# Performance work log

Hardware: AMD Instinct MI355X
Metric: run time of the kernel (lower is better)

## Reference

```python
import jax, jax.numpy as jnp
import numpy as np

EPS = 1e-6
R_ROTS = 3
MAX_DEG = 4.0
MD = 1  # max_disp_z = max_disp_y = max_disp_x = 1
E = (2 * MD + 1) ** 3  # 27


def eul2rotm_y(ry):
    # rotation about the y axis (rx = rz = 0 in the original eul2rotm call)
    c, s = jnp.cos(ry), jnp.sin(ry)
    z, o = jnp.zeros_like(ry), jnp.ones_like(ry)
    return jnp.stack([jnp.stack([c, z, s], -1),
                      jnp.stack([z, o, z], -1),
                      jnp.stack([-s, z, c], -1)], -2)  # [N,3,3]


def merge_rt(r, t):
    N = r.shape[0]
    top = jnp.concatenate([r, t[:, :, None]], axis=2)
    bot = jnp.broadcast_to(jnp.array([[[0.0, 0.0, 0.0, 1.0]]], dtype=r.dtype), (N, 1, 4))
    return jnp.concatenate([top, bot], axis=1)  # [N,4,4]


def invert_rt(rt):
    r = rt[:, :3, :3]
    t = rt[:, :3, 3]
    rinv = jnp.swapaxes(r, 1, 2)
    tinv = -jnp.einsum('nij,nj->ni', rinv, t)
    return merge_rt(rinv, tinv)


def trilinear_sample(vox, xyz):
    # vox [N,C,Z,Y,X]; xyz [N,Z,Y,X,3] voxel-space (x,y,z) coords; zero outside
    N, C, Z, Y, X = vox.shape
    x, y, z = xyz[..., 0], xyz[..., 1], xyz[..., 2]
    x0, y0, z0 = jnp.floor(x), jnp.floor(y), jnp.floor(z)
    fx, fy, fz = x - x0, y - y0, z - z0
    voxf = vox.reshape(N, C, Z * Y * X)
    gather = jax.vmap(lambda v, i: v[:, i])  # per-batch gather over flat spatial
    out = jnp.zeros((N, C, Z, Y, X), vox.dtype)
    for dz in (0, 1):
        wz = fz if dz else (1.0 - fz)
        zc = z0 + dz
        for dy in (0, 1):
            wy = fy if dy else (1.0 - fy)
            yc = y0 + dy
            for dx in (0, 1):
                wx = fx if dx else (1.0 - fx)
                xc = x0 + dx
                valid = ((xc >= 0) & (xc <= X - 1) & (yc >= 0) & (yc <= Y - 1)
                         & (zc >= 0) & (zc <= Z - 1))
                xi = jnp.clip(xc, 0, X - 1).astype(jnp.int32)
                yi = jnp.clip(yc, 0, Y - 1).astype(jnp.int32)
                zi = jnp.clip(zc, 0, Z - 1).astype(jnp.int32)
                idx = (zi * Y + yi) * X + xi  # [N,Z,Y,X]
                vals = gather(voxf, idx.reshape(N, -1)).reshape(N, C, Z, Y, X)
                w = (wx * wy * wz * valid.astype(vox.dtype))[:, None]
                out = out + w * vals
    return out


def apply_4x4_to_vox(T, vox):
    # warp vox by rigid transform T (unit voxel size, grid-centered Mem2Ref)
    N, C, Z, Y, X = vox.shape
    Tinv = invert_rt(T)
    zz, yy, xx = jnp.meshgrid(jnp.arange(Z), jnp.arange(Y), jnp.arange(X), indexing='ij')
    grid = jnp.stack([xx, yy, zz], -1).astype(vox.dtype)  # [Z,Y,X,3] in (x,y,z)
    center = (jnp.array([X, Y, Z], vox.dtype) - 1.0) / 2.0
    ref = grid - center
    src = jnp.einsum('nij,zyxj->nzyxi', Tinv[:, :3, :3], ref) + Tinv[:, None, None, None, :3, 3]
    return trilinear_sample(vox, src + center)


def cost_volume_3d(v0, v1):
    # masked-mean correlation over C for every shift in a 3x3x3 neighborhood
    N, C, D, H, W = v0.shape
    v1p = jnp.pad(v1, ((0, 0), (0, 0), (MD, MD), (MD, MD), (MD, MD)))
    mask = jnp.pad(jnp.ones((N, 1, D, H, W), v0.dtype),
                   ((0, 0), (0, 0), (MD, MD), (MD, MD), (MD, MD)))
    costs = []
    for dz in range(2 * MD + 1):
        for dy in range(2 * MD + 1):
            for dx in range(2 * MD + 1):
                sl = v1p[:, :, dz:dz + D, dy:dy + H, dx:dx + W]
                m = mask[:, :, dz:dz + D, dy:dy + H, dx:dx + W]
                num = jnp.sum(v0 * sl, axis=1, keepdims=True)
                den = m * C  # sum of mask broadcast over C channels
                costs.append(num / (den + EPS))
    return jnp.concatenate(costs, axis=1)  # [N,27,D,H,W]


def setup_inputs() -> dict:
    key = jax.random.key(0)
    ks = jax.random.split(key, 8)
    B, C, Z, Y, X = 4, 32, 64, 32, 64
    feat0 = jax.random.normal(ks[0], (B, C, Z, Y, X), jnp.float32)
    feat1 = jax.random.normal(ks[1], (B, C, Z, Y, X), jnp.float32)
    ry_g = jax.random.uniform(ks[2], (B,), jnp.float32, -0.05, 0.05)
    t_g = 0.5 * jax.random.normal(ks[3], (B, 3), jnp.float32)
    cam0_T_cam1_g = merge_rt(eul2rotm_y(ry_g), t_g)
    fan = R_ROTS * E  # 81
    W1 = jax.random.normal(ks[4], (128, fan), jnp.float32) / np.sqrt(fan)
    b1 = jnp.zeros((128,), jnp.float32)
    W2 = jax.random.normal(ks[5], (128, 128), jnp.float32) / np.sqrt(128.0)
    b2 = jnp.zeros((128,), jnp.float32)
    W3 = jax.random.normal(ks[6], (4, 128), jnp.float32) / np.sqrt(128.0)
    b3 = jnp.zeros((4,), jnp.float32)
    return dict(feat0=feat0, feat1=feat1, cam0_T_cam1_g=cam0_T_cam1_g,
                W1=W1, b1=b1, W2=W2, b2=b2, W3=W3, b3=b3)


def reference(feat0, feat1, cam0_T_cam1_g, W1, b1, W2, b2, W3, b3):
    B, C, Z, Y, X = feat0.shape
    # candidate y-rotations, replicated per batch element
    rots = jnp.linspace(-MAX_DEG, MAX_DEG, R_ROTS)
    ry = jnp.tile(rots[None, :], (B, 1)).reshape(B * R_ROTS)
    camN_T_cam1 = merge_rt(eul2rotm_y(jnp.deg2rad(ry)), jnp.zeros((B * R_ROTS, 3), feat0.dtype))
    feat0r = jnp.repeat(feat0[:, None], R_ROTS, axis=1).reshape(B * R_ROTS, C, Z, Y, X)
    feat1r = jnp.repeat(feat1[:, None], R_ROTS, axis=1).reshape(B * R_ROTS, C, Z, Y, X)
    featN = apply_4x4_to_vox(camN_T_cam1, feat1r)
    cc = cost_volume_3d(feat0r, featN)                # [B*R,27,Z,Y,X]
    heat = jnp.sum(cc, axis=(2, 3, 4))                 # [B*R,27]
    f = heat.reshape(B, R_ROTS * E)
    f = jax.nn.leaky_relu(f, 0.1)
    f = f / (EPS + jnp.sqrt(jnp.sum(f * f, axis=1, keepdims=True)))
    f = jax.nn.leaky_relu(f @ W1.T + b1, 0.1)
    f = jax.nn.leaky_relu(f @ W2.T + b2, 0.1)
    f = f @ W3.T + b3                                  # [B,4]
    r_out, yv, xv, zv = f[:, 0], f[:, 1], f[:, 2], f[:, 3]
    # Mem2Ref is affine with unit voxel size -> delta == (x,y,z) directly
    delta = jnp.stack([xv, yv, zv], axis=1)
    cam0_T_cam1_e = merge_rt(eul2rotm_y(jnp.deg2rad(r_out)), -delta)
    feat1_warped = apply_4x4_to_vox(cam0_T_cam1_e, feat1)
    # eval_against_gt (coeffs folded to 1.0, sc=1.0)
    ry_of = lambda rt: jnp.arctan2(rt[:, 0, 2], rt[:, 2, 2])
    deg_e = jnp.rad2deg(ry_of(cam0_T_cam1_e))
    deg_g = jnp.rad2deg(ry_of(cam0_T_cam1_g))
    t_e = cam0_T_cam1_e[:, :3, 3]
    t_g = cam0_T_cam1_g[:, :3, 3]
    t_l2 = jnp.mean(jnp.sum((t_e - t_g) ** 2, axis=1))
    deg_l2 = jnp.mean((deg_e - deg_g) ** 2)
    total_loss = t_l2 + deg_l2
    return total_loss, cam0_T_cam1_e, feat1_warped
```

## Files before the change

### kernel.cpp

```cpp
#include <hip/hip_runtime.h>
#include <math.h>

#define NCH 32
#define CHV (64*32*64)
#define NB 4
#define NT2 512
#define INVC (1.0f/(32.0f+1e-6f))
#define D2R 0.017453292519943295f
#define R2D 57.29577951308232f

#define P1A 73
#define P1B 72
#define F0B (32*P1A)
#define UNITSZ (32*P1A + 24*P1B)

__global__ __launch_bounds__(256) void k_heat(const float* __restrict__ feat0,
                                              const float* __restrict__ feat1,
                                              float* __restrict__ partial)
{
    __shared__ float L[2][UNITSZ];

    const int lid = (int)blockIdx.x;
    const int nid = (lid & 7) * 256 + (lid >> 3);
    const int yt  = nid & 7;
    const int zt  = (nid >> 3) & 31;
    const int chh = (nid >> 8) & 1;
    const int b   = nid >> 9;

    const int tid = (int)threadIdx.x;
    const int wv = tid >> 6;
    const int lane = tid & 63;
    const int tx = lane & 15, ty = lane >> 4;
    const int x0 = 4 * tx;
    const int z0 = 2 * zt;
    const bool ident = (wv == 1);

    const float* f0base = feat0 + ((size_t)b * NCH + chh * 16) * CHV;
    const float* f1base = feat1 + ((size_t)b * NCH + chh * 16) * CHV;

    int aB[2][4];
    float wAx[2][4], wBx[2][4], wZl[2][4];
    if (wv == 0 || wv == 2) {
        const float th = 4.0f * (float)(wv - 1) * D2R;
        const float cs = cosf(th), sn = sinf(th);
        #pragma unroll
        for (int k = 0; k < 2; ++k) {
            #pragma unroll
            for (int i = 0; i < 4; ++i) {
                const float rx = (float)(x0 + i) - 31.5f;
                const float rz = (float)(z0 + k) - 31.5f;
                const float sx = cs * rx - sn * rz + 31.5f;
                const float sz = sn * rx + cs * rz + 31.5f;
                const float xf = floorf(sx), zf = floorf(sz);
                const float fx = sx - xf, fz = sz - zf;
                const int ix = (int)xf, iz = (int)zf;
                int bx; float A_, B_;
                if (ix == -1)      { bx = 0;  A_ = fx;        B_ = 0.0f; }
                else if (ix == 63) { bx = 62; A_ = 0.0f;      B_ = 1.0f - fx; }
                else if ((unsigned)ix <= 62u) { bx = ix; A_ = 1.0f - fx; B_ = fx; }
                else               { bx = 0;  A_ = 0.0f;      B_ = 0.0f; }
                wAx[k][i] = A_; wBx[k][i] = B_;
                wZl[k][i] = 1.0f - fz;
                const int zl = min(max(iz - (2 * zt - 3), 0), 6);
                aB[k][i] = (zl * 4 + ty) * P1A + bx;
            }
        }
    }
    const int iA0 = (12 + ty) * P1A + x0;
    const int iA1 = iA0 + 4 * P1A;
    const int fb0 = F0B + ty * P1B + x0;

    float acc[27];
    #pragma unroll
    for (int o = 0; o < 27; ++o) acc[o] = 0.0f;

#define STAGE_CH(CHN)                                                           \
    {                                                                           \
        const int u_ = (CHN) & 1;                                               \
        const float* f1c_ = f1base + (size_t)(CHN) * CHV;                       \
        const float* f0c_ = f0base + (size_t)(CHN) * CHV;                       \
        float* Ln_ = &L[u_][0];                                                 \
        const int tq_ = lane >> 4, c4_ = (lane & 15) << 2;                      \
        float4 v1_[8], v0_[6];                                                  \
        _Pragma("unroll")                                                       \
        for (int k_ = 0; k_ < 8; ++k_) {                                        \
            const int zs_ = 2 * zt - 3 + k_;                                    \
            v1_[k_] = (float4){0.0f, 0.0f, 0.0f, 0.0f};                         \
            if (zs_ >= 0 && zs_ < 64)                                           \
                v1_[k_] = *(const float4*)(f1c_ + zs_ * 2048                    \
                            + (4 * yt + tq_) * 64 + c4_);                       \
        }                                                                       \
        _Pragma("unroll")                                                       \
        for (int k_ = 0; k_ < 6; ++k_) {                                        \
            const int r_ = 4 * k_ + tq_;                                        \
            const int i_ = (r_ * 43) >> 8;                                      \
            const int j_ = r_ - 6 * i_;                                         \
            const int zf_ = 2 * zt - 1 + i_;                                    \
            const int yf_ = 4 * yt - 1 + j_;                                    \
            v0_[k_] = (float4){0.0f, 0.0f, 0.0f, 0.0f};                         \
            if (zf_ >= 0 && zf_ < 64 && yf_ >= 0 && yf_ < 32)                   \
                v0_[k_] = *(const float4*)(f0c_ + zf_ * 2048 + yf_ * 64 + c4_); \
        }                                                                       \
        _Pragma("unroll")                                                       \
        for (int k_ = 0; k_ < 8; ++k_) {                                        \
            const int w_ = (4 * k_ + tq_) * P1A + c4_;                          \
            Ln_[w_ + 0] = v1_[k_].x; Ln_[w_ + 1] = v1_[k_].y;                   \
            Ln_[w_ + 2] = v1_[k_].z; Ln_[w_ + 3] = v1_[k_].w;                   \
        }                                                                       \
        _Pragma("unroll")                                                       \
        for (int k_ = 0; k_ < 6; ++k_)                                          \
            *(float4*)&Ln_[F0B + (4 * k_ + tq_) * P1B + c4_] = v0_[k_];         \
    }

#define ROWFMA(KK, OZP1, YRI, R)                                                \
    { const int base_ = (OZP1) * 9 + (2 - (YRI)) * 3;                           \
      acc[base_ + 0] += g0[KK]*R.x + fr[KK][0]*R.y + fr[KK][1]*R.z + fr[KK][2]*R.w; \
      acc[base_ + 1] += fr[KK][0]*R.x + fr[KK][1]*R.y + fr[KK][2]*R.z + fr[KK][3]*R.w; \
      acc[base_ + 2] += fr[KK][1]*R.x + fr[KK][2]*R.y + fr[KK][3]*R.z + g5[KK]*R.w; }

    if (wv == 3) STAGE_CH(0)
    __syncthreads();

    #pragma unroll 1
    for (int ch = 0; ch < 16; ++ch) {
        if (wv == 3) {
            if (ch + 1 < 16) STAGE_CH(ch + 1)
        } else {
            const float* Lb = &L[ch & 1][0];

            float fr[2][4];
            if (ident) {
                #pragma unroll
                for (int i = 0; i < 4; ++i) {
                    fr[0][i] = Lb[iA0 + i];
                    fr[1][i] = Lb[iA1 + i];
                }
            } else {
                #pragma unroll
                for (int k = 0; k < 2; ++k) {
                    #pragma unroll
                    for (int i = 0; i < 4; ++i) {
                        const int a = aB[k][i];
                        const float p00 = Lb[a], p01 = Lb[a + 1];
                        const float p10 = Lb[a + 4 * P1A], p11 = Lb[a + 4 * P1A + 1];
                        const float sLo = wAx[k][i] * p00 + wBx[k][i] * p01;
                        const float sHi = wAx[k][i] * p10 + wBx[k][i] * p11;
                        fr[k][i] = sHi + wZl[k][i] * (sLo - sHi);
                    }
                }
            }

            float g0[2], g5[2];
            #pragma unroll
            for (int k = 0; k < 2; ++k) {
                const float a_ = __shfl_up(fr[k][3], 1, 64);
                const float c_ = __shfl_down(fr[k][0], 1, 64);
                g0[k] = (tx == 0) ? 0.0f : a_;
                g5[k] = (tx == 15) ? 0.0f : c_;
            }

            __builtin_amdgcn_s_setprio(1);
            #pragma unroll
            for (int zri = 0; zri < 4; ++zri) {
                const float4 R0 = *(const float4*)&Lb[fb0 + (zri * 6 + 0) * P1B];
                const float4 R1 = *(const float4*)&Lb[fb0 + (zri * 6 + 1) * P1B];
                const float4 R2 = *(const float4*)&Lb[fb0 + (zri * 6 + 2) * P1B];
                if (zri == 0) { ROWFMA(0, 2, 0, R0) ROWFMA(0, 2, 1, R1) ROWFMA(0, 2, 2, R2) }
                if (zri == 1) { ROWFMA(0, 1, 0, R0) ROWFMA(0, 1, 1, R1) ROWFMA(0, 1, 2, R2)
                                ROWFMA(1, 2, 0, R0) ROWFMA(1, 2, 1, R1) ROWFMA(1, 2, 2, R2) }
                if (zri == 2) { ROWFMA(0, 0, 0, R0) ROWFMA(0, 0, 1, R1) ROWFMA(0, 0, 2, R2)
                                ROWFMA(1, 1, 0, R0) ROWFMA(1, 1, 1, R1) ROWFMA(1, 1, 2, R2) }
                if (zri == 3) { ROWFMA(1, 0, 0, R0) ROWFMA(1, 0, 1, R1) ROWFMA(1, 0, 2, R2) }
            }
            __builtin_amdgcn_s_setprio(0);
        }
        __syncthreads();
    }
#undef ROWFMA
#undef STAGE_CH

    if (wv < 3) {
        const int slot = (zt * 8 + yt) * 2 + chh;
        #pragma unroll 1
        for (int o = 0; o < 27; ++o) {
            float v = acc[o];
            #pragma unroll
            for (int d = 32; d >= 1; d >>= 1) v += __shfl_down(v, d, 64);
            if (lane == 0)
                partial[((size_t)((b * 3 + wv) * 27) + o) * NT2 + slot] = v;
        }
    }
}

__global__ __launch_bounds__(128) void k_hsum(const float* __restrict__ partial,
                                              float* __restrict__ heatw)
{
    __shared__ float red[2];
    const int r = (int)blockIdx.x;
    const int tid = (int)threadIdx.x;
    const int lane = tid & 63, wid = tid >> 6;

    const float4 v = ((const float4*)(partial + (size_t)r * NT2))[tid];
    float s = (v.x + v.y) + (v.z + v.w);
    #pragma unroll
    for (int d = 32; d >= 1; d >>= 1) s += __shfl_down(s, d, 64);
    if (lane == 0) red[wid] = s;
    __syncthreads();
    if (tid == 0) heatw[r] = (red[0] + red[1]) * INVC;
}

__global__ __launch_bounds__(128) void k_mlp(const float* __restrict__ heatw,
                                             const float* __restrict__ camg,
                                             const float* __restrict__ W1,
                                             const float* __restrict__ b1,
                                             const float* __restrict__ W2,
                                             const float* __restrict__ b2,
                                             const float* __restrict__ W3,
                                             const float* __restrict__ b3,
                                             float* __restrict__ out,
                                             float* __restrict__ params)
{
    __shared__ float heat[324];
    __shared__ float f[81];
    __shared__ float h1[128];
    __shared__ float h2[128];
    __shared__ float denom_s;
    __shared__ float res[NB][8];
    const int tid = (int)threadIdx.x;

    for (int p = tid; p < 324; p += 128) heat[p] = heatw[p];
    __syncthreads();

    for (int b = 0; b < NB; ++b) {
        if (tid < 81) {
            float v = heat[b * 81 + tid];
            f[tid] = (v >= 0.0f) ? v : 0.1f * v;
        }
        __syncthreads();
        if (tid == 0) {
            float ss = 0.0f;
            for (int k = 0; k < 81; ++k) ss += f[k] * f[k];
            denom_s = 1e-6f + sqrtf(ss);
        }
        __syncthreads();
        if (tid < 81) f[tid] = f[tid] / denom_s;
        __syncthreads();
        {
            float a = b1[tid];
            const float* wr = W1 + tid * 81;
            for (int k = 0; k < 81; ++k) a += wr[k] * f[k];
            h1[tid] = (a >= 0.0f) ? a : 0.1f * a;
        }
        __syncthreads();
        {
            float a = b2[tid];
            const float* wr = W2 + tid * 128;
            for (int k = 0; k < 128; ++k) a += wr[k] * h1[k];
            h2[tid] = (a >= 0.0f) ? a : 0.1f * a;
        }
        __syncthreads();
        if (tid < 4) {
            float a = b3[tid];
            const float* wr = W3 + tid * 128;
            for (int k = 0; k < 128; ++k) a += wr[k] * h2[k];
            res[b][4 + tid] = a;
        }
        __syncthreads();
        if (tid == 0) {
            const float r_out = res[b][4], yv = res[b][5], xv = res[b][6], zv = res[b][7];
            const float t2 = r_out * D2R;
            const float c2 = cosf(t2), s2 = sinf(t2);
            float* m = out + 1 + b * 16;
            m[0] = c2;  m[1] = 0.0f; m[2] = s2;  m[3] = -xv;
            m[4] = 0.0f; m[5] = 1.0f; m[6] = 0.0f; m[7] = -yv;
            m[8] = -s2; m[9] = 0.0f; m[10] = c2; m[11] = -zv;
            m[12] = 0.0f; m[13] = 0.0f; m[14] = 0.0f; m[15] = 1.0f;
            params[b * 8 + 0] = c2;
            params[b * 8 + 1] = s2;
            params[b * 8 + 2] = c2 * xv - s2 * zv;
            params[b * 8 + 3] = yv;
            params[b * 8 + 4] = s2 * xv + c2 * zv;
            res[b][0] = -xv; res[b][1] = -yv; res[b][2] = -zv;
            res[b][3] = atan2f(s2, c2) * R2D;
        }
        __syncthreads();
    }

    if (tid == 0) {
        float tl2 = 0.0f, dl2 = 0.0f;
        for (int b = 0; b < NB; ++b) {
            const float* g = camg + b * 16;
            const float dx = res[b][0] - g[3];
            const float dy = res[b][1] - g[7];
            const float dz = res[b][2] - g[11];
            tl2 += dx * dx + dy * dy + dz * dz;
            const float dg = atan2f(g[2], g[10]) * R2D;
            const float dd = res[b][3] - dg;
            dl2 += dd * dd;
        }
        out[0] = tl2 * 0.25f + dl2 * 0.25f;
    }
}

__global__ __launch_bounds__(256) void k_warp(const float* __restrict__ feat1,
                                              const float* __restrict__ params,
                                              float* __restrict__ outw)
{
    const int b = blockIdx.y;
    const int p = (int)blockIdx.x * 256 + (int)threadIdx.x;
    const int z = p >> 11;
    const int y = (p >> 6) & 31;
    const int x = p & 63;

    const float cs = params[b * 8 + 0], sn = params[b * 8 + 1];
    const float tpx = params[b * 8 + 2], tpy = params[b * 8 + 3], tpz = params[b * 8 + 4];

    const float rx = (float)x - 31.5f;
    const float ry = (float)y - 15.5f;
    const float rz = (float)z - 31.5f;
    const float sx = cs * rx - sn * rz + tpx + 31.5f;
    const float sy = ry + tpy + 15.5f;
    const float sz = sn * rx + cs * rz + tpz + 31.5f;

    const float xf = floorf(sx), yf = floorf(sy), zf = floorf(sz);
    const float fx = sx - xf, fy = sy - yf, fz = sz - zf;
    const int ix = (int)xf, iy = (int)yf, iz = (int)zf;

    const float wx[2] = {1.0f - fx, fx};
    const float wy[2] = {1.0f - fy, fy};
    const float wz[2] = {1.0f - fz, fz};
    const int xs[2] = {min(max(ix, 0), 63), min(max(ix + 1, 0), 63)};
    const int ys[2] = {min(max(iy, 0), 31), min(max(iy + 1, 0), 31)};
    const int zs[2] = {min(max(iz, 0), 63), min(max(iz + 1, 0), 63)};
    const bool vx[2] = {(unsigned)ix < 64u, (unsigned)(ix + 1) < 64u};
    const bool vy[2] = {(unsigned)iy < 32u, (unsigned)(iy + 1) < 32u};
    const bool vz[2] = {(unsigned)iz < 64u, (unsigned)(iz + 1) < 64u};

    int idx[8]; float w[8];
    int q = 0;
    #pragma unroll
    for (int dz = 0; dz < 2; ++dz)
        #pragma unroll
        for (int dy = 0; dy < 2; ++dy)
            #pragma unroll
            for (int dx = 0; dx < 2; ++dx) {
                idx[q] = zs[dz] * 2048 + ys[dy] * 64 + xs[dx];
                w[q] = (vx[dx] && vy[dy] && vz[dz]) ? wx[dx] * wy[dy] * wz[dz] : 0.0f;
                ++q;
            }

    const float* f1b = feat1 + (size_t)b * NCH * CHV;
    float* ob = outw + (size_t)b * NCH * CHV;
    #pragma unroll 2
    for (int c = 0; c < NCH; ++c) {
        const float* f1c = f1b + (size_t)c * CHV;
        float a = 0.0f;
        #pragma unroll
        for (int k = 0; k < 8; ++k) a += w[k] * f1c[idx[k]];
        ob[(size_t)c * CHV + p] = a;
    }
}

extern "C" void kernel_launch(void* const* d_in, const int* in_sizes, int n_in,
                              void* d_out, int out_size, void* d_ws, size_t ws_size,
                              hipStream_t stream)
{
    (void)in_sizes; (void)n_in; (void)out_size; (void)ws_size;
    const float* feat0 = (const float*)d_in[0];
    const float* feat1 = (const float*)d_in[1];
    const float* camg  = (const float*)d_in[2];
    const float* W1 = (const float*)d_in[3];
    const float* b1 = (const float*)d_in[4];
    const float* W2 = (const float*)d_in[5];
    const float* b2 = (const float*)d_in[6];
    const float* W3 = (const float*)d_in[7];
    const float* b3 = (const float*)d_in[8];
    float* out = (float*)d_out;

    float* partial = (float*)d_ws;
    float* params  = partial + 324 * NT2;
    float* heatw   = params + 32;

    hipLaunchKernelGGL(k_heat, dim3(2048), dim3(256), 0, stream,
                       feat0, feat1, partial);
    hipLaunchKernelGGL(k_hsum, dim3(324), dim3(128), 0, stream, partial, heatw);
    hipLaunchKernelGGL(k_mlp, dim3(1), dim3(128), 0, stream,
                       heatw, camg, W1, b1, W2, b2, W3, b3, out, params);
    dim3 g3((64*32*64) / 256, NB);
    hipLaunchKernelGGL(k_warp, g3, dim3(256), 0, stream, feat1, params, out + 65);
}
```

Measured before the change: 192.6 us.

## Fuse heat reduction into per-batch MLP, split loss, vectorize warp

Removes the separate partial-sum reduction kernel and folds it into the MLP kernel, which now runs one block per batch, so the four batches no longer run serially in a single block. The final loss moves into a tiny separate kernel. The warp kernel now handles four consecutive x voxels per thread, writes them with a float4 store, and remaps blocks to spread batches across XCDs. The priority hints around the FMA section of k_heat are also dropped. The per-thread loop over 128 float4 in the MLP block is a serial read that could lengthen that stage.

Result: slower. 274.8 us (+42.7%).

```diff
diff --git a/kernel.cpp b/kernel.cpp
--- a/kernel.cpp
+++ b/kernel.cpp
@@ -159,7 +159,6 @@
                 g5[k] = (tx == 15) ? 0.0f : c_;
             }
 
-            __builtin_amdgcn_s_setprio(1);
             #pragma unroll
             for (int zri = 0; zri < 4; ++zri) {
                 const float4 R0 = *(const float4*)&Lb[fb0 + (zri * 6 + 0) * P1B];
@@ -172,7 +171,6 @@
                                 ROWFMA(1, 1, 0, R0) ROWFMA(1, 1, 1, R1) ROWFMA(1, 1, 2, R2) }
                 if (zri == 3) { ROWFMA(1, 0, 0, R0) ROWFMA(1, 0, 1, R1) ROWFMA(1, 0, 2, R2) }
             }
-            __builtin_amdgcn_s_setprio(0);
         }
         __syncthreads();
     }
@@ -192,25 +190,7 @@
     }
 }
 
-__global__ __launch_bounds__(128) void k_hsum(const float* __restrict__ partial,
-                                              float* __restrict__ heatw)
-{
-    __shared__ float red[2];
-    const int r = (int)blockIdx.x;
-    const int tid = (int)threadIdx.x;
-    const int lane = tid & 63, wid = tid >> 6;
-
-    const float4 v = ((const float4*)(partial + (size_t)r * NT2))[tid];
-    float s = (v.x + v.y) + (v.z + v.w);
-    #pragma unroll
-    for (int d = 32; d >= 1; d >>= 1) s += __shfl_down(s, d, 64);
-    if (lane == 0) red[wid] = s;
-    __syncthreads();
-    if (tid == 0) heatw[r] = (red[0] + red[1]) * INVC;
-}
-
-__global__ __launch_bounds__(128) void k_mlp(const float* __restrict__ heatw,
-                                             const float* __restrict__ camg,
+__global__ __launch_bounds__(128) void k_mlp(const float* __restrict__ partial,
                                              const float* __restrict__ W1,
                                              const float* __restrict__ b1,
                                              const float* __restrict__ W2,
@@ -218,84 +198,93 @@
                                              const float* __restrict__ W3,
                                              const float* __restrict__ b3,
                                              float* __restrict__ out,
-                                             float* __restrict__ params)
-{
-    __shared__ float heat[324];
+                                             float* __restrict__ params,
+                                             float* __restrict__ resv)
+{
     __shared__ float f[81];
     __shared__ float h1[128];
     __shared__ float h2[128];
     __shared__ float denom_s;
-    __shared__ float res[NB][8];
+    __shared__ float r4[4];
+    const int b = (int)blockIdx.x;
     const int tid = (int)threadIdx.x;
 
-    for (int p = tid; p < 324; p += 128) heat[p] = heatw[p];
-    __syncthreads();
-
-    for (int b = 0; b < NB; ++b) {
-        if (tid < 81) {
-            float v = heat[b * 81 + tid];
-            f[tid] = (v >= 0.0f) ? v : 0.1f * v;
-        }
-        __syncthreads();
-        if (tid == 0) {
-            float ss = 0.0f;
-            for (int k = 0; k < 81; ++k) ss += f[k] * f[k];
-            denom_s = 1e-6f + sqrtf(ss);
-        }
-        __syncthreads();
-        if (tid < 81) f[tid] = f[tid] / denom_s;
-        __syncthreads();
-        {
-            float a = b1[tid];
-            const float* wr = W1 + tid * 81;
-            for (int k = 0; k < 81; ++k) a += wr[k] * f[k];
-            h1[tid] = (a >= 0.0f) ? a : 0.1f * a;
-        }
-        __syncthreads();
-        {
-            float a = b2[tid];
-            const float* wr = W2 + tid * 128;
-            for (int k = 0; k < 128; ++k) a += wr[k] * h1[k];
-            h2[tid] = (a >= 0.0f) ? a : 0.1f * a;
-        }
-        __syncthreads();
-        if (tid < 4) {
-            float a = b3[tid];
-            const float* wr = W3 + tid * 128;
-            for (int k = 0; k < 128; ++k) a += wr[k] * h2[k];
-            res[b][4 + tid] = a;
-        }
-        __syncthreads();
-        if (tid == 0) {
-            const float r_out = res[b][4], yv = res[b][5], xv = res[b][6], zv = res[b][7];
-            const float t2 = r_out * D2R;
-            const float c2 = cosf(t2), s2 = sinf(t2);
-            float* m = out + 1 + b * 16;
-            m[0] = c2;  m[1] = 0.0f; m[2] = s2;  m[3] = -xv;
-            m[4] = 0.0f; m[5] = 1.0f; m[6] = 0.0f; m[7] = -yv;
-            m[8] = -s2; m[9] = 0.0f; m[10] = c2; m[11] = -zv;
-            m[12] = 0.0f; m[13] = 0.0f; m[14] = 0.0f; m[15] = 1.0f;
-            params[b * 8 + 0] = c2;
-            params[b * 8 + 1] = s2;
-            params[b * 8 + 2] = c2 * xv - s2 * zv;
-            params[b * 8 + 3] = yv;
-            params[b * 8 + 4] = s2 * xv + c2 * zv;
-            res[b][0] = -xv; res[b][1] = -yv; res[b][2] = -zv;
-            res[b][3] = atan2f(s2, c2) * R2D;
-        }
-        __syncthreads();
-    }
-
+    if (tid < 81) {
+        const float4* p = (const float4*)(partial + ((size_t)b * 81 + tid) * NT2);
+        float s0 = 0.f, s1 = 0.f, s2 = 0.f, s3 = 0.f;
+        #pragma unroll 4
+        for (int i = 0; i < NT2 / 4; ++i) {
+            const float4 v = p[i];
+            s0 += v.x; s1 += v.y; s2 += v.z; s3 += v.w;
+        }
+        const float hv = ((s0 + s1) + (s2 + s3)) * INVC;
+        f[tid] = (hv >= 0.0f) ? hv : 0.1f * hv;
+    }
+    __syncthreads();
     if (tid == 0) {
+        float ss = 0.0f;
+        for (int k = 0; k < 81; ++k) ss += f[k] * f[k];
+        denom_s = 1e-6f + sqrtf(ss);
+    }
+    __syncthreads();
+    if (tid < 81) f[tid] = f[tid] / denom_s;
+    __syncthreads();
+    {
+        float a = b1[tid];
+        const float* wr = W1 + tid * 81;
+        for (int k = 0; k < 81; ++k) a += wr[k] * f[k];
+        h1[tid] = (a >= 0.0f) ? a : 0.1f * a;
+    }
+    __syncthreads();
+    {
+        float a = b2[tid];
+        const float* wr = W2 + tid * 128;
+        for (int k = 0; k < 128; ++k) a += wr[k] * h1[k];
+        h2[tid] = (a >= 0.0f) ? a : 0.1f * a;
+    }
+    __syncthreads();
+    if (tid < 4) {
+        float a = b3[tid];
+        const float* wr = W3 + tid * 128;
+        for (int k = 0; k < 128; ++k) a += wr[k] * h2[k];
+        r4[tid] = a;
+    }
+    __syncthreads();
+    if (tid == 0) {
+        const float r_out = r4[0], yv = r4[1], xv = r4[2], zv = r4[3];
+        const float t2 = r_out * D2R;
+        const float c2 = cosf(t2), s2 = sinf(t2);
+        float* m = out + 1 + b * 16;
+        m[0] = c2;  m[1] = 0.0f; m[2] = s2;  m[3] = -xv;
+        m[4] = 0.0f; m[5] = 1.0f; m[6] = 0.0f; m[7] = -yv;
+        m[8] = -s2; m[9] = 0.0f; m[10] = c2; m[11] = -zv;
+        m[12] = 0.0f; m[13] = 0.0f; m[14] = 0.0f; m[15] = 1.0f;
+        params[b * 8 + 0] = c2;
+        params[b * 8 + 1] = s2;
+        params[b * 8 + 2] = c2 * xv - s2 * zv;
+        params[b * 8 + 3] = yv;
+        params[b * 8 + 4] = s2 * xv + c2 * zv;
+        resv[b * 4 + 0] = -xv;
+        resv[b * 4 + 1] = -yv;
+        resv[b * 4 + 2] = -zv;
+        resv[b * 4 + 3] = atan2f(s2, c2) * R2D;
+    }
+}
+
+__global__ __launch_bounds__(64) void k_loss(const float* __restrict__ resv,
+                                             const float* __restrict__ camg,
+                                             float* __restrict__ out)
+{
+    if (threadIdx.x == 0) {
         float tl2 = 0.0f, dl2 = 0.0f;
         for (int b = 0; b < NB; ++b) {
             const float* g = camg + b * 16;
-            const float dx = res[b][0] - g[3];
-            const float dy = res[b][1] - g[7];
-            const float dz = res[b][2] - g[11];
+            const float dx = resv[b * 4 + 0] - g[3];
+            const float dy = resv[b * 4 + 1] - g[7];
+            const float dz = resv[b * 4 + 2] - g[11];
             tl2 += dx * dx + dy * dy + dz * dz;
             const float dg = atan2f(g[2], g[10]) * R2D;
-            const float dd = res[b][3] - dg;
+            const float dd = resv[b * 4 + 3] - dg;
             dl2 += dd * dd;
         }
         out[0] = tl2 * 0.25f + dl2 * 0.25f;
@@ -306,58 +295,74 @@
                                               const float* __restrict__ params,
                                               float* __restrict__ outw)
 {
-    const int b = blockIdx.y;
-    const int p = (int)blockIdx.x * 256 + (int)threadIdx.x;
-    const int z = p >> 11;
-    const int y = (p >> 6) & 31;
-    const int x = p & 63;
+    const int flat = (int)blockIdx.y * 128 + (int)blockIdx.x;
+    const int nid = (flat & 7) * 64 + (flat >> 3);
+    const int b = nid >> 7;
+    const int pblk = nid & 127;
+
+    const int tid = (int)threadIdx.x;
+    const int p0 = (pblk * 256 + tid) * 4;
+    const int z = p0 >> 11;
+    const int y = (p0 >> 6) & 31;
+    const int x0 = p0 & 63;
 
     const float cs = params[b * 8 + 0], sn = params[b * 8 + 1];
     const float tpx = params[b * 8 + 2], tpy = params[b * 8 + 3], tpz = params[b * 8 + 4];
 
-    const float rx = (float)x - 31.5f;
     const float ry = (float)y - 15.5f;
     const float rz = (float)z - 31.5f;
-    const float sx = cs * rx - sn * rz + tpx + 31.5f;
     const float sy = ry + tpy + 15.5f;
-    const float sz = sn * rx + cs * rz + tpz + 31.5f;
-
-    const float xf = floorf(sx), yf = floorf(sy), zf = floorf(sz);
-    const float fx = sx - xf, fy = sy - yf, fz = sz - zf;
-    const int ix = (int)xf, iy = (int)yf, iz = (int)zf;
-
-    const float wx[2] = {1.0f - fx, fx};
+    const float yf = floorf(sy);
+    const float fy = sy - yf;
+    const int iy = (int)yf;
     const float wy[2] = {1.0f - fy, fy};
-    const float wz[2] = {1.0f - fz, fz};
-    const int xs[2] = {min(max(ix, 0), 63), min(max(ix + 1, 0), 63)};
     const int ys[2] = {min(max(iy, 0), 31), min(max(iy + 1, 0), 31)};
-    const int zs[2] = {min(max(iz, 0), 63), min(max(iz + 1, 0), 63)};
-    const bool vx[2] = {(unsigned)ix < 64u, (unsigned)(ix + 1) < 64u};
     const bool vy[2] = {(unsigned)iy < 32u, (unsigned)(iy + 1) < 32u};
-    const bool vz[2] = {(unsigned)iz < 64u, (unsigned)(iz + 1) < 64u};
-
-    int idx[8]; float w[8];
-    int q = 0;
+
+    int idx[4][8]; float w[4][8];
     #pragma unroll
-    for (int dz = 0; dz < 2; ++dz)
+    for (int i = 0; i < 4; ++i) {
+        const float rx = (float)(x0 + i) - 31.5f;
+        const float sx = cs * rx - sn * rz + tpx + 31.5f;
+        const float sz = sn * rx + cs * rz + tpz + 31.5f;
+        const float xf = floorf(sx), zf = floorf(sz);
+        const float fx = sx - xf, fz = sz - zf;
+        const int ix = (int)xf, iz = (int)zf;
+        const float wx[2] = {1.0f - fx, fx};
+        const float wz[2] = {1.0f - fz, fz};
+        const int xs[2] = {min(max(ix, 0), 63), min(max(ix + 1, 0), 63)};
+        const int zs[2] = {min(max(iz, 0), 63), min(max(iz + 1, 0), 63)};
+        const bool vx[2] = {(unsigned)ix < 64u, (unsigned)(ix + 1) < 64u};
+        const bool vz[2] = {(unsigned)iz < 64u, (unsigned)(iz + 1) < 64u};
+        int q = 0;
         #pragma unroll
-        for (int dy = 0; dy < 2; ++dy)
-            #pragma unroll
-            for (int dx = 0; dx < 2; ++dx) {
-                idx[q] = zs[dz] * 2048 + ys[dy] * 64 + xs[dx];
-                w[q] = (vx[dx] && vy[dy] && vz[dz]) ? wx[dx] * wy[dy] * wz[dz] : 0.0f;
-                ++q;
-            }
+        for (int dz = 0; dz < 2; ++dz)
+            #pragma unroll
+            for (int dy = 0; dy < 2; ++dy)
+                #pragma unroll
+                for (int dx = 0; dx < 2; ++dx) {
+                    idx[i][q] = zs[dz] * 2048 + ys[dy] * 64 + xs[dx];
+                    w[i][q] = (vx[dx] && vy[dy] && vz[dz])
+                              ? wx[dx] * wy[dy] * wz[dz] : 0.0f;
+                    ++q;
+                }
+    }
 
     const float* f1b = feat1 + (size_t)b * NCH * CHV;
     float* ob = outw + (size_t)b * NCH * CHV;
-    #pragma unroll 2
+    #pragma unroll 1
     for (int c = 0; c < NCH; ++c) {
         const float* f1c = f1b + (size_t)c * CHV;
-        float a = 0.0f;
+        float4 r;
+        float* rp = (float*)&r;
         #pragma unroll
-        for (int k = 0; k < 8; ++k) a += w[k] * f1c[idx[k]];
-        ob[(size_t)c * CHV + p] = a;
+        for (int i = 0; i < 4; ++i) {
+            float a = 0.0f;
+            #pragma unroll
+            for (int k = 0; k < 8; ++k) a += w[i][k] * f1c[idx[i][k]];
+            rp[i] = a;
+        }
+        *(float4*)(ob + (size_t)c * CHV + p0) = r;
     }
 }
 
@@ -379,13 +384,13 @@
 
     float* partial = (float*)d_ws;
     float* params  = partial + 324 * NT2;
-    float* heatw   = params + 32;
+    float* resv    = params + 32;
 
     hipLaunchKernelGGL(k_heat, dim3(2048), dim3(256), 0, stream,
                        feat0, feat1, partial);
-    hipLaunchKernelGGL(k_hsum, dim3(324), dim3(128), 0, stream, partial, heatw);
-    hipLaunchKernelGGL(k_mlp, dim3(1), dim3(128), 0, stream,
-                       heatw, camg, W1, b1, W2, b2, W3, b3, out, params);
-    dim3 g3((64*32*64) / 256, NB);
-    hipLaunchKernelGGL(k_warp, g3, dim3(256), 0, stream, feat1, params, out + 65);
-}
+    hipLaunchKernelGGL(k_mlp, dim3(4), dim3(128), 0, stream,
+                       partial, W1, b1, W2, b2, W3, b3, out, params, resv);
+    hipLaunchKernelGGL(k_loss, dim3(1), dim3(64), 0, stream, resv, camg, out);
+    hipLaunchKernelGGL(k_warp, dim3(128, 4), dim3(256), 0, stream,
+                       feat1, params, out + 65);
+}
```
